# Optimization experiments

Hardware: AMD Instinct MI355X
Metric: run time of the kernel (lower is better)

The kernel has to match this reference:

```python
import jax, jax.numpy as jnp
import numpy as np

N_NODE = 2000
N_EDGE = 100000
N_REL2 = 102  # num_relation * 2
D_IN = 64
N_TRI = 500000


def _triangles(src, dst, N):
    """Faithful numpy port of triangle_list: for each edge (a,c) intersect
    out-neighbors of a with in-neighbors of c via sorted edge lists + searchsorted.
    Returns (edge_ab, edge_bc, edge_ac) edge-index triples."""
    E = len(src)
    src = src.astype(np.int64); dst = dst.astype(np.int64)
    in_order = np.argsort(src * N + dst, kind='stable')   # edges sorted by (a,b)
    out_order = np.argsort(dst * N + src, kind='stable')  # edges sorted by (c,b)
    deg_in = np.bincount(src, minlength=N)
    deg_out = np.bincount(dst, minlength=N)
    neighbor_out = dst[in_order]
    neighbor_in = src[out_order]
    cum_in = np.concatenate([[0], np.cumsum(deg_in)])
    cum_out = np.concatenate([[0], np.cumsum(deg_out)])
    # candidate b's: out-neighbors of a, replicated per edge (a,c)
    cnt_a = deg_in[src]
    ce = np.repeat(np.arange(E), cnt_a)
    offs = np.arange(cnt_a.sum()) - np.repeat(np.cumsum(cnt_a) - cnt_a, cnt_a)
    pos = np.repeat(cum_in[src], cnt_a) + offs
    b = neighbor_out[pos]
    ab_cand = in_order[pos]
    # boundary: in-neighbors of c, replicated per edge (globally sorted via N*segment offset)
    cnt_c = deg_out[dst]
    se = np.repeat(np.arange(E), cnt_c)
    offs2 = np.arange(cnt_c.sum()) - np.repeat(np.cumsum(cnt_c) - cnt_c, cnt_c)
    pos2 = np.repeat(cum_out[dst], cnt_c) + offs2
    boundary = neighbor_in[pos2] + N * se
    bc_order = out_order[pos2]
    key = b + N * ce
    left = np.searchsorted(boundary, key, side='left')
    right = np.searchsorted(boundary, key, side='right')
    count = right - left
    rep = np.repeat(np.arange(len(count)), count)
    within = np.arange(count.sum()) - np.repeat(np.cumsum(count) - count, count)
    return ab_cand[rep], bc_order[left[rep] + within], ce[rep]


def setup_inputs() -> dict:
    rng = np.random.default_rng(0)
    src = rng.integers(0, N_NODE, N_EDGE)
    dst = rng.integers(0, N_NODE, N_EDGE)
    edge_type = rng.integers(0, N_REL2, N_EDGE)
    ab, bc, ac = _triangles(src, dst, N_NODE)
    if len(ab) == 0:  # pathological fallback
        ab = rng.integers(0, N_EDGE, N_TRI)
        bc = rng.integers(0, N_EDGE, N_TRI)
        ac = rng.integers(0, N_EDGE, N_TRI)
    sel = rng.integers(0, len(ab), N_TRI)  # fixed-size (re)sample of triangles
    s = 0.1
    return {
        'edge_type': jnp.asarray(edge_type, jnp.int64) if jax.config.jax_enable_x64 else jnp.asarray(edge_type, jnp.int32),
        'edge_ab': jnp.asarray(ab[sel], jnp.int32),
        'edge_bc': jnp.asarray(bc[sel], jnp.int32),
        'edge_ac': jnp.asarray(ac[sel], jnp.int32),
        'fact_emb': jnp.asarray(rng.standard_normal((N_REL2, D_IN)) * s, jnp.float32),
        'W1': jnp.asarray(rng.standard_normal((D_IN, D_IN)) * s, jnp.float32),
        'b1': jnp.zeros((D_IN,), jnp.float32),
        'W2': jnp.asarray(rng.standard_normal((D_IN, D_IN)) * s, jnp.float32),
        'b2': jnp.zeros((D_IN,), jnp.float32),
        'mlp_W1': jnp.asarray(rng.standard_normal((2 * D_IN, 2 * D_IN)) * s, jnp.float32),
        'mlp_b1': jnp.zeros((2 * D_IN,), jnp.float32),
        'mlp_W2': jnp.asarray(rng.standard_normal((2 * D_IN, 1)) * s, jnp.float32),
        'mlp_b2': jnp.zeros((1,), jnp.float32),
    }


def reference(edge_type, edge_ab, edge_bc, edge_ac, fact_emb,
              W1, b1, W2, b2, mlp_W1, mlp_b1, mlp_W2, mlp_b2):
    E = edge_type.shape[0]
    x0 = fact_emb[edge_type]                      # [E, d] initial edge (fact) features
    x = x0
    for W, b in ((W1, b1), (W2, b2)):
        msg = x[edge_ab] * x[edge_bc]             # [T, d] distmult triangle messages
        agg = jax.ops.segment_sum(msg, edge_ac, num_segments=E)  # scatter-add onto ac edge
        x = jax.nn.relu(agg @ W + b)              # per-layer linear + activation
    feat = jnp.concatenate([x, x0], axis=-1)      # [E, 2d] (hidden + input, concat_hidden=False)
    h = jax.nn.relu(feat @ mlp_W1 + mlp_b1)
    return (h @ mlp_W2 + mlp_b2)[:, 0]            # [E] per-edge score
```

## Files before the change

kernel.cpp:

```cpp
#include <hip/hip_runtime.h>

#define D 64

__device__ __forceinline__ float relu_f(float v) { return v > 0.f ? v : 0.f; }


__global__ void k_hist(const int* __restrict__ ac, int* __restrict__ cnt, int T) {
    int t = blockIdx.x * blockDim.x + threadIdx.x;
    if (t < T) atomicAdd(&cnt[ac[t]], 1);
}

__global__ __launch_bounds__(256) void k_scanA(const int* __restrict__ cnt,
        int* __restrict__ localExcl, int* __restrict__ blockSums, int E) {
    __shared__ int ls[256];
    const int tid = threadIdx.x;
    int base = blockIdx.x * 1024 + tid * 4;
    int a0 = 0, a1 = 0, a2 = 0, a3 = 0;
    if (base + 3 < E) {
        int4 v = *reinterpret_cast<const int4*>(cnt + base);
        a0 = v.x; a1 = v.y; a2 = v.z; a3 = v.w;
    } else {
        if (base + 0 < E) a0 = cnt[base + 0];
        if (base + 1 < E) a1 = cnt[base + 1];
        if (base + 2 < E) a2 = cnt[base + 2];
        if (base + 3 < E) a3 = cnt[base + 3];
    }
    int tsum = a0 + a1 + a2 + a3;
    ls[tid] = tsum;
    __syncthreads();
    for (int off = 1; off < 256; off <<= 1) {
        int v = (tid >= off) ? ls[tid - off] : 0;
        __syncthreads();
        ls[tid] += v;
        __syncthreads();
    }
    int excl = ls[tid] - tsum;
    if (tid == 255) blockSums[blockIdx.x] = ls[255];
    if (base + 3 < E) {
        int4 o = make_int4(excl, excl + a0, excl + a0 + a1, excl + a0 + a1 + a2);
        *reinterpret_cast<int4*>(localExcl + base) = o;
    } else {
        int run = excl;
        if (base + 0 < E) { localExcl[base + 0] = run; run += a0; }
        if (base + 1 < E) { localExcl[base + 1] = run; run += a1; }
        if (base + 2 < E) { localExcl[base + 2] = run; run += a2; }
        if (base + 3 < E) { localExcl[base + 3] = run; }
    }
}

__global__ __launch_bounds__(256) void k_scanC(const int* __restrict__ localExcl,
        const int* __restrict__ blockSums, const int* __restrict__ cnt,
        int2* __restrict__ seg, int* __restrict__ cursor, int E, int nblk) {
    __shared__ int ls[256];
    const int tid = threadIdx.x;
    int v = (tid < nblk) ? blockSums[tid] : 0;
    ls[tid] = v;
    __syncthreads();
    for (int off = 1; off < 256; off <<= 1) {
        int w = (tid >= off) ? ls[tid - off] : 0;
        __syncthreads();
        ls[tid] += w;
        __syncthreads();
    }
    int excl = ls[tid] - v;
    __syncthreads();
    ls[tid] = excl;
    __syncthreads();
    int i = blockIdx.x * blockDim.x + tid;
    if (i < E) {
        int s = localExcl[i] + ls[i >> 10];
        seg[i] = make_int2(s, cnt[i]);
        cursor[i] = s;
    }
}

__global__ void k_permute(const int* __restrict__ ab, const int* __restrict__ bc,
                          const int* __restrict__ ac, const int* __restrict__ et,
                          int* __restrict__ cursor, int2* __restrict__ tri,
                          int* __restrict__ pid, int T, int nrel) {
    int t = blockIdx.x * blockDim.x + threadIdx.x;
    if (t >= T) return;
    int a = ab[t], b = bc[t];
    int pos = atomicAdd(&cursor[ac[t]], 1);
    tri[pos] = make_int2(a, b);
    pid[pos] = et[a] * nrel + et[b];
}

#define FPAD 65
__global__ __launch_bounds__(256) void k_pair(const float* __restrict__ fe,
        const float* __restrict__ W1, float* __restrict__ P, int nrel) {
    __shared__ float Wl[64 * 64];
    __shared__ float fT[64 * FPAD];
    const int npair = nrel * nrel;
    const int tid = threadIdx.x;
    const int p0 = blockIdx.x * 64;

    for (int i = tid; i < 1024; i += 256)
        reinterpret_cast<float4*>(Wl)[i] = reinterpret_cast<const float4*>(W1)[i];

    for (int i = tid; i < 1024; i += 256) {
        int r = i >> 4, q = i & 15;
        int p = p0 + r;
        float4 v = make_float4(0.f, 0.f, 0.f, 0.f);
        if (p < npair) {
            int pa = p / nrel, pb = p - pa * nrel;
            float4 va = reinterpret_cast<const float4*>(fe + (size_t)pa * D)[q];
            float4 vb = reinterpret_cast<const float4*>(fe + (size_t)pb * D)[q];
            v = make_float4(va.x * vb.x, va.y * vb.y, va.z * vb.z, va.w * vb.w);
        }
        fT[(q * 4 + 0) * FPAD + r] = v.x;
        fT[(q * 4 + 1) * FPAD + r] = v.y;
        fT[(q * 4 + 2) * FPAD + r] = v.z;
        fT[(q * 4 + 3) * FPAD + r] = v.w;
    }
    __syncthreads();

    const int j0 = (tid & 15) * 4;
    const int r0 = (tid >> 4) * 4;
    float acc[4][4];
    #pragma unroll
    for (int i = 0; i < 4; ++i)
        #pragma unroll
        for (int j = 0; j < 4; ++j) acc[i][j] = 0.f;

    #pragma unroll 8
    for (int k = 0; k < 64; ++k) {
        float4 f = *reinterpret_cast<const float4*>(&fT[k * FPAD + r0]);
        float4 w = *reinterpret_cast<const float4*>(&Wl[k * 64 + j0]);
        float fa[4] = {f.x, f.y, f.z, f.w};
        float wa[4] = {w.x, w.y, w.z, w.w};
        #pragma unroll
        for (int i = 0; i < 4; ++i)
            #pragma unroll
            for (int j = 0; j < 4; ++j) acc[i][j] += fa[i] * wa[j];
    }

    #pragma unroll
    for (int i = 0; i < 4; ++i) {
        int p = p0 + r0 + i;
        if (p < npair) {
            float4 o = make_float4(acc[i][0], acc[i][1], acc[i][2], acc[i][3]);
            *reinterpret_cast<float4*>(P + (size_t)p * D + j0) = o;
        }
    }
}

__global__ __launch_bounds__(128) void k_qtab(const float* __restrict__ fe,
        const float* __restrict__ mW1, const float* __restrict__ mb1,
        float* __restrict__ Q) {
    __shared__ float fl[64];
    const int t = blockIdx.x;
    const int j = threadIdx.x;
    if (j < 64) fl[j] = fe[(size_t)t * D + j];
    __syncthreads();
    float s = mb1[j];
    #pragma unroll 16
    for (int k = 0; k < 64; ++k)
        s += fl[k] * mW1[(size_t)(64 + k) * 128 + j];
    Q[(size_t)t * 128 + j] = s;
}

__global__ __launch_bounds__(256) void k_msg1b(const int2* __restrict__ seg,
        const int* __restrict__ pid, const float* __restrict__ P,
        const float* __restrict__ b1, float* __restrict__ xb, int E, int nquad) {
    const int tid = threadIdx.x;
    const int lane = tid & 63;
    const int sub = lane & 15;
    const int grp = lane >> 4;
    const float4* __restrict__ P4 = reinterpret_cast<const float4*>(P);
    const float4 bb = reinterpret_cast<const float4*>(b1)[sub];

    for (int quad = (blockIdx.x * blockDim.x + tid) >> 6; quad * 4 < E; quad += nquad) {
        const int e = quad * 4 + grp;
        int2 sc = make_int2(0, 0);
        if (e < E) sc = seg[e];
        const int s = sc.x, c = sc.y;
        float4 acc = make_float4(0.f, 0.f, 0.f, 0.f);
        int i = 0;
        for (; i + 3 < c; i += 4) {
            int q0 = pid[s + i + 0];
            int q1 = pid[s + i + 1];
            int q2 = pid[s + i + 2];
            int q3 = pid[s + i + 3];
            float4 v0 = P4[(size_t)q0 * 16 + sub];
            float4 v1 = P4[(size_t)q1 * 16 + sub];
            float4 v2 = P4[(size_t)q2 * 16 + sub];
            float4 v3 = P4[(size_t)q3 * 16 + sub];
            acc.x += v0.x + v1.x + v2.x + v3.x;
            acc.y += v0.y + v1.y + v2.y + v3.y;
            acc.z += v0.z + v1.z + v2.z + v3.z;
            acc.w += v0.w + v1.w + v2.w + v3.w;
        }
        for (; i < c; ++i) {
            float4 v = P4[(size_t)pid[s + i] * 16 + sub];
            acc.x += v.x; acc.y += v.y; acc.z += v.z; acc.w += v.w;
        }
        if (e < E) {
            float4 o;
            o.x = relu_f(acc.x + bb.x);
            o.y = relu_f(acc.y + bb.y);
            o.z = relu_f(acc.z + bb.z);
            o.w = relu_f(acc.w + bb.w);
            reinterpret_cast<float4*>(xb + (size_t)e * D)[sub] = o;
        }
    }
}

__global__ __launch_bounds__(256) void k_msg4(const int2* __restrict__ seg,
        const int2* __restrict__ tri, const float* __restrict__ xin,
        float* __restrict__ agg, int E, int nquad) {
    const int tid = threadIdx.x;
    const int lane = tid & 63;
    const int sub = lane & 15;
    const int grp = lane >> 4;
    const float4* __restrict__ x4 = reinterpret_cast<const float4*>(xin);

    for (int quad = (blockIdx.x * blockDim.x + tid) >> 6; quad * 4 < E; quad += nquad) {
        const int e = quad * 4 + grp;
        int2 sc = make_int2(0, 0);
        if (e < E) sc = seg[e];
        const int s = sc.x, c = sc.y;
        float4 acc = make_float4(0.f, 0.f, 0.f, 0.f);
        int i = 0;
        for (; i + 3 < c; i += 4) {
            int2 p0 = tri[s + i + 0];
            int2 p1 = tri[s + i + 1];
            int2 p2 = tri[s + i + 2];
            int2 p3 = tri[s + i + 3];
            float4 va0 = x4[(size_t)p0.x * 16 + sub];
            float4 vb0 = x4[(size_t)p0.y * 16 + sub];
            float4 va1 = x4[(size_t)p1.x * 16 + sub];
            float4 vb1 = x4[(size_t)p1.y * 16 + sub];
            float4 va2 = x4[(size_t)p2.x * 16 + sub];
            float4 vb2 = x4[(size_t)p2.y * 16 + sub];
            float4 va3 = x4[(size_t)p3.x * 16 + sub];
            float4 vb3 = x4[(size_t)p3.y * 16 + sub];
            acc.x += va0.x * vb0.x; acc.y += va0.y * vb0.y;
            acc.z += va0.z * vb0.z; acc.w += va0.w * vb0.w;
            acc.x += va1.x * vb1.x; acc.y += va1.y * vb1.y;
            acc.z += va1.z * vb1.z; acc.w += va1.w * vb1.w;
            acc.x += va2.x * vb2.x; acc.y += va2.y * vb2.y;
            acc.z += va2.z * vb2.z; acc.w += va2.w * vb2.w;
            acc.x += va3.x * vb3.x; acc.y += va3.y * vb3.y;
            acc.z += va3.z * vb3.z; acc.w += va3.w * vb3.w;
        }
        for (; i < c; ++i) {
            int2 p = tri[s + i];
            float4 va = x4[(size_t)p.x * 16 + sub];
            float4 vb = x4[(size_t)p.y * 16 + sub];
            acc.x += va.x * vb.x;
            acc.y += va.y * vb.y;
            acc.z += va.z * vb.z;
            acc.w += va.w * vb.w;
        }
        if (e < E)
            reinterpret_cast<float4*>(agg + (size_t)e * D)[sub] = acc;
    }
}

__global__ __launch_bounds__(256) void k_linear(const float* __restrict__ in,
        const float* __restrict__ W, const float* __restrict__ b,
        float* __restrict__ outx, int E) {
    __shared__ float Wl[64 * 64];
    __shared__ float fT[64 * FPAD];
    const int tid = threadIdx.x;
    const int row0 = blockIdx.x * 64;

    for (int i = tid; i < 1024; i += 256)
        reinterpret_cast<float4*>(Wl)[i] = reinterpret_cast<const float4*>(W)[i];

    for (int i = tid; i < 1024; i += 256) {
        int r = i >> 4, q = i & 15;
        float4 v = make_float4(0.f, 0.f, 0.f, 0.f);
        if (row0 + r < E)
            v = reinterpret_cast<const float4*>(in + (size_t)(row0 + r) * D)[q];
        fT[(q * 4 + 0) * FPAD + r] = v.x;
        fT[(q * 4 + 1) * FPAD + r] = v.y;
        fT[(q * 4 + 2) * FPAD + r] = v.z;
        fT[(q * 4 + 3) * FPAD + r] = v.w;
    }
    __syncthreads();

    const int j0 = (tid & 15) * 4;
    const int r0 = (tid >> 4) * 4;
    float acc[4][4];
    #pragma unroll
    for (int i = 0; i < 4; ++i)
        #pragma unroll
        for (int j = 0; j < 4; ++j) acc[i][j] = 0.f;

    #pragma unroll 8
    for (int k = 0; k < 64; ++k) {
        float4 f = *reinterpret_cast<const float4*>(&fT[k * FPAD + r0]);
        float4 w = *reinterpret_cast<const float4*>(&Wl[k * 64 + j0]);
        float fa[4] = {f.x, f.y, f.z, f.w};
        float wa[4] = {w.x, w.y, w.z, w.w};
        #pragma unroll
        for (int i = 0; i < 4; ++i)
            #pragma unroll
            for (int j = 0; j < 4; ++j) acc[i][j] += fa[i] * wa[j];
    }

    float4 bv = *reinterpret_cast<const float4*>(&b[j0]);
    float ba[4] = {bv.x, bv.y, bv.z, bv.w};
    #pragma unroll
    for (int i = 0; i < 4; ++i) {
        int row = row0 + r0 + i;
        if (row < E) {
            float4 o;
            o.x = relu_f(acc[i][0] + ba[0]);
            o.y = relu_f(acc[i][1] + ba[1]);
            o.z = relu_f(acc[i][2] + ba[2]);
            o.w = relu_f(acc[i][3] + ba[3]);
            *reinterpret_cast<float4*>(outx + (size_t)row * D + j0) = o;
        }
    }
}

#define MPAD 129
__global__ __launch_bounds__(512) void k_mlp(const float* __restrict__ x,
        const int* __restrict__ et, const float* __restrict__ Q,
        const float* __restrict__ W1, const float* __restrict__ W2,
        const float* __restrict__ b2, float* __restrict__ out, int E) {
    __shared__ float Wl[32 * 128];
    __shared__ float fT[32 * MPAD];
    __shared__ float W2l[128];
    const int tid = threadIdx.x;
    const int row0 = blockIdx.x * 128;

    if (tid < 128) W2l[tid] = W2[tid];

    const int jt = tid & 31;
    const int j0 = jt * 4;
    const int r0 = (tid >> 5) * 8;
    float acc[8][4];
    #pragma unroll
    for (int i = 0; i < 8; ++i)
        #pragma unroll
        for (int j = 0; j < 4; ++j) acc[i][j] = 0.f;

    for (int h = 0; h < 2; ++h) {
        __syncthreads();
        for (int i = tid; i < 1024; i += 512)
            reinterpret_cast<float4*>(Wl)[i] =
                reinterpret_cast<const float4*>(W1 + (size_t)h * 32 * 128)[i];
        for (int i = tid; i < 1024; i += 512) {
            int r = i >> 3, q = i & 7;
            int row = row0 + r;
            float4 v = make_float4(0.f, 0.f, 0.f, 0.f);
            if (row < E)
                v = reinterpret_cast<const float4*>(x + (size_t)row * D)[h * 8 + q];
            int kb = q * 4;
            fT[(kb + 0) * MPAD + r] = v.x;
            fT[(kb + 1) * MPAD + r] = v.y;
            fT[(kb + 2) * MPAD + r] = v.z;
            fT[(kb + 3) * MPAD + r] = v.w;
        }
        __syncthreads();

        #pragma unroll 4
        for (int k = 0; k < 32; ++k) {
            float4 fA = *reinterpret_cast<const float4*>(&fT[k * MPAD + r0]);
            float4 fB = *reinterpret_cast<const float4*>(&fT[k * MPAD + r0 + 4]);
            float4 w = *reinterpret_cast<const float4*>(&Wl[k * 128 + j0]);
            float fa[8] = {fA.x, fA.y, fA.z, fA.w, fB.x, fB.y, fB.z, fB.w};
            float wa[4] = {w.x, w.y, w.z, w.w};
            #pragma unroll
            for (int i = 0; i < 8; ++i)
                #pragma unroll
                for (int j = 0; j < 4; ++j) acc[i][j] += fa[i] * wa[j];
        }
    }

    float4 w2 = *reinterpret_cast<const float4*>(&W2l[j0]);
    float bias2 = b2[0];
    #pragma unroll
    for (int i = 0; i < 8; ++i) {
        int row = row0 + r0 + i;
        float4 qv = make_float4(0.f, 0.f, 0.f, 0.f);
        if (row < E)
            qv = reinterpret_cast<const float4*>(Q + (size_t)et[row] * 128)[jt];
        float h0 = relu_f(acc[i][0] + qv.x);
        float h1 = relu_f(acc[i][1] + qv.y);
        float h2 = relu_f(acc[i][2] + qv.z);
        float h3 = relu_f(acc[i][3] + qv.w);
        float p = h0 * w2.x + h1 * w2.y + h2 * w2.z + h3 * w2.w;
        #pragma unroll
        for (int m = 1; m < 32; m <<= 1) p += __shfl_xor(p, m, 64);
        if (jt == 0 && row < E) out[row] = p + bias2;
    }
}

extern "C" void kernel_launch(void* const* d_in, const int* in_sizes, int n_in,
                              void* d_out, int out_size, void* d_ws, size_t ws_size,
                              hipStream_t stream) {
    const int*   edge_type = (const int*)d_in[0];
    const int*   ab        = (const int*)d_in[1];
    const int*   bc        = (const int*)d_in[2];
    const int*   ac        = (const int*)d_in[3];
    const float* fe        = (const float*)d_in[4];
    const float* W1        = (const float*)d_in[5];
    const float* b1        = (const float*)d_in[6];
    const float* W2        = (const float*)d_in[7];
    const float* b2        = (const float*)d_in[8];
    const float* mW1       = (const float*)d_in[9];
    const float* mb1       = (const float*)d_in[10];
    const float* mW2       = (const float*)d_in[11];
    const float* mb2       = (const float*)d_in[12];

    const int E = in_sizes[0];
    const int T = in_sizes[1];
    const int nrel = in_sizes[4] / D;
    const int npair = nrel * nrel;
    float* out = (float*)d_out;

    char* p = (char*)d_ws;
    float* xa   = (float*)p;   p += (size_t)E * D * sizeof(float);
    float* xb   = (float*)p;   p += (size_t)E * D * sizeof(float);
    float* agg  = (float*)p;   p += (size_t)E * D * sizeof(float);
    float* P    = (float*)p;   p += (size_t)npair * D * sizeof(float);
    float* Q    = (float*)p;   p += (size_t)nrel * 128 * sizeof(float);
    int* cnt    = (int*)p;     p += (size_t)E * sizeof(int);
    int* lexcl  = (int*)p;     p += (size_t)E * sizeof(int);
    int* cursor = (int*)p;     p += (size_t)E * sizeof(int);
    int* bsums  = (int*)p;     p += 256 * sizeof(int);
    int2* seg   = (int2*)p;    p += (size_t)E * sizeof(int2);
    int2* tri   = (int2*)p;    p += (size_t)T * sizeof(int2);
    int* pid    = (int*)p;     p += (size_t)T * sizeof(int);

    const int nblkA = (E + 1023) / 1024;

    hipMemsetAsync(cnt, 0, (size_t)E * sizeof(int), stream);
    k_hist<<<(T + 255) / 256, 256, 0, stream>>>(ac, cnt, T);
    k_pair<<<(npair + 63) / 64, 256, 0, stream>>>(fe, W1, P, nrel);
    k_qtab<<<nrel, 128, 0, stream>>>(fe, mW1, mb1, Q);
    k_scanA<<<nblkA, 256, 0, stream>>>(cnt, lexcl, bsums, E);
    k_scanC<<<(E + 255) / 256, 256, 0, stream>>>(lexcl, bsums, cnt, seg, cursor, E, nblkA);
    k_permute<<<(T + 255) / 256, 256, 0, stream>>>(ab, bc, ac, edge_type, cursor, tri, pid, T, nrel);

    const int MSG_BLOCKS = 2048;
    const int nquad = MSG_BLOCKS * 256 / 64;
    k_msg1b<<<MSG_BLOCKS, 256, 0, stream>>>(seg, pid, P, b1, xb, E, nquad);
    k_msg4<<<MSG_BLOCKS, 256, 0, stream>>>(seg, tri, xb, agg, E, nquad);
    k_linear<<<(E + 63) / 64, 256, 0, stream>>>(agg, W2, b2, xa, E);

    k_mlp<<<(E + 127) / 128, 512, 0, stream>>>(xa, edge_type, Q, mW1, mW2, mb2, out, E);
}
```

Measured before the change: 182.9 us.

## Fuse setup kernels into one prep launch and merge layer-2 linear with MLP

Replaces the memset, pair-table and Q-table launches with a single block-partitioned prep kernel. It also fuses the second-layer linear with the final MLP, so the hidden activations stay in shared memory instead of being written to and re-read from a global buffer. This removes three launches and one E×64 float round trip through global memory. In exchange the fused kernel runs extra sequential GEMM phases with more syncs per block, and uses 64-row tiles instead of the previous 128-row MLP tiles.

Result: faster. 164.4 us (-10.2%).

```diff
diff --git a/kernel.cpp b/kernel.cpp
--- a/kernel.cpp
+++ b/kernel.cpp
@@ -1,8 +1,98 @@
 #include <hip/hip_runtime.h>
 
 #define D 64
+#define FPAD 65
 
 __device__ __forceinline__ float relu_f(float v) { return v > 0.f ? v : 0.f; }
+
+__global__ __launch_bounds__(256) void k_prep(int* __restrict__ cnt, int En,
+        const float* __restrict__ fe, const float* __restrict__ W1,
+        float* __restrict__ P, int nrel,
+        const float* __restrict__ mW1, const float* __restrict__ mb1,
+        float* __restrict__ Q, int nZ, int nP) {
+    __shared__ float Wl[64 * 64];
+    __shared__ float fT[64 * FPAD];
+    const int tid = threadIdx.x;
+    int b = blockIdx.x;
+
+    if (b < nZ) {
+        int i = (b * 256 + tid) * 4;
+        if (i + 3 < En) {
+            *reinterpret_cast<int4*>(cnt + i) = make_int4(0, 0, 0, 0);
+        } else {
+            for (int k = i; k < En; ++k) cnt[k] = 0;
+        }
+        return;
+    }
+    b -= nZ;
+    if (b < nP) {
+        const int npair = nrel * nrel;
+        const int p0 = b * 64;
+
+        for (int i = tid; i < 1024; i += 256)
+            reinterpret_cast<float4*>(Wl)[i] = reinterpret_cast<const float4*>(W1)[i];
+
+        for (int i = tid; i < 1024; i += 256) {
+            int r = i >> 4, q = i & 15;
+            int p = p0 + r;
+            float4 v = make_float4(0.f, 0.f, 0.f, 0.f);
+            if (p < npair) {
+                int pa = p / nrel, pb = p - pa * nrel;
+                float4 va = reinterpret_cast<const float4*>(fe + (size_t)pa * D)[q];
+                float4 vb = reinterpret_cast<const float4*>(fe + (size_t)pb * D)[q];
+                v = make_float4(va.x * vb.x, va.y * vb.y, va.z * vb.z, va.w * vb.w);
+            }
+            fT[(q * 4 + 0) * FPAD + r] = v.x;
+            fT[(q * 4 + 1) * FPAD + r] = v.y;
+            fT[(q * 4 + 2) * FPAD + r] = v.z;
+            fT[(q * 4 + 3) * FPAD + r] = v.w;
+        }
+        __syncthreads();
+
+        const int j0 = (tid & 15) * 4;
+        const int r0 = (tid >> 4) * 4;
+        float acc[4][4];
+        #pragma unroll
+        for (int i = 0; i < 4; ++i)
+            #pragma unroll
+            for (int j = 0; j < 4; ++j) acc[i][j] = 0.f;
+
+        #pragma unroll 8
+        for (int k = 0; k < 64; ++k) {
+            float4 f = *reinterpret_cast<const float4*>(&fT[k * FPAD + r0]);
+            float4 w = *reinterpret_cast<const float4*>(&Wl[k * 64 + j0]);
+            float fa[4] = {f.x, f.y, f.z, f.w};
+            float wa[4] = {w.x, w.y, w.z, w.w};
+            #pragma unroll
+            for (int i = 0; i < 4; ++i)
+                #pragma unroll
+                for (int j = 0; j < 4; ++j) acc[i][j] += fa[i] * wa[j];
+        }
+
+        #pragma unroll
+        for (int i = 0; i < 4; ++i) {
+            int p = p0 + r0 + i;
+            if (p < npair) {
+                float4 o = make_float4(acc[i][0], acc[i][1], acc[i][2], acc[i][3]);
+                *reinterpret_cast<float4*>(P + (size_t)p * D + j0) = o;
+            }
+        }
+        return;
+    }
+    b -= nP;
+    int t = b * 2 + (tid >> 7);
+    int j = tid & 127;
+    float* fl = &fT[(tid >> 7) * 64];
+    if (t < nrel && j < 64) fl[j] = fe[(size_t)t * D + j];
+    __syncthreads();
+    if (t < nrel) {
+        float s = mb1[j];
+        #pragma unroll 16
+        for (int k = 0; k < 64; ++k)
+            s += fl[k] * mW1[(size_t)(64 + k) * 128 + j];
+        Q[(size_t)t * 128 + j] = s;
+    }
+}
 
 
 __global__ void k_hist(const int* __restrict__ ac, int* __restrict__ cnt, int T) {
@@ -84,80 +174,6 @@
     int pos = atomicAdd(&cursor[ac[t]], 1);
     tri[pos] = make_int2(a, b);
     pid[pos] = et[a] * nrel + et[b];
-}
-
-#define FPAD 65
-__global__ __launch_bounds__(256) void k_pair(const float* __restrict__ fe,
-        const float* __restrict__ W1, float* __restrict__ P, int nrel) {
-    __shared__ float Wl[64 * 64];
-    __shared__ float fT[64 * FPAD];
-    const int npair = nrel * nrel;
-    const int tid = threadIdx.x;
-    const int p0 = blockIdx.x * 64;
-
-    for (int i = tid; i < 1024; i += 256)
-        reinterpret_cast<float4*>(Wl)[i] = reinterpret_cast<const float4*>(W1)[i];
-
-    for (int i = tid; i < 1024; i += 256) {
-        int r = i >> 4, q = i & 15;
-        int p = p0 + r;
-        float4 v = make_float4(0.f, 0.f, 0.f, 0.f);
-        if (p < npair) {
-            int pa = p / nrel, pb = p - pa * nrel;
-            float4 va = reinterpret_cast<const float4*>(fe + (size_t)pa * D)[q];
-            float4 vb = reinterpret_cast<const float4*>(fe + (size_t)pb * D)[q];
-            v = make_float4(va.x * vb.x, va.y * vb.y, va.z * vb.z, va.w * vb.w);
-        }
-        fT[(q * 4 + 0) * FPAD + r] = v.x;
-        fT[(q * 4 + 1) * FPAD + r] = v.y;
-        fT[(q * 4 + 2) * FPAD + r] = v.z;
-        fT[(q * 4 + 3) * FPAD + r] = v.w;
-    }
-    __syncthreads();
-
-    const int j0 = (tid & 15) * 4;
-    const int r0 = (tid >> 4) * 4;
-    float acc[4][4];
-    #pragma unroll
-    for (int i = 0; i < 4; ++i)
-        #pragma unroll
-        for (int j = 0; j < 4; ++j) acc[i][j] = 0.f;
-
-    #pragma unroll 8
-    for (int k = 0; k < 64; ++k) {
-        float4 f = *reinterpret_cast<const float4*>(&fT[k * FPAD + r0]);
-        float4 w = *reinterpret_cast<const float4*>(&Wl[k * 64 + j0]);
-        float fa[4] = {f.x, f.y, f.z, f.w};
-        float wa[4] = {w.x, w.y, w.z, w.w};
-        #pragma unroll
-        for (int i = 0; i < 4; ++i)
-            #pragma unroll
-            for (int j = 0; j < 4; ++j) acc[i][j] += fa[i] * wa[j];
-    }
-
-    #pragma unroll
-    for (int i = 0; i < 4; ++i) {
-        int p = p0 + r0 + i;
-        if (p < npair) {
-            float4 o = make_float4(acc[i][0], acc[i][1], acc[i][2], acc[i][3]);
-            *reinterpret_cast<float4*>(P + (size_t)p * D + j0) = o;
-        }
-    }
-}
-
-__global__ __launch_bounds__(128) void k_qtab(const float* __restrict__ fe,
-        const float* __restrict__ mW1, const float* __restrict__ mb1,
-        float* __restrict__ Q) {
-    __shared__ float fl[64];
-    const int t = blockIdx.x;
-    const int j = threadIdx.x;
-    if (j < 64) fl[j] = fe[(size_t)t * D + j];
-    __syncthreads();
-    float s = mb1[j];
-    #pragma unroll 16
-    for (int k = 0; k < 64; ++k)
-        s += fl[k] * mW1[(size_t)(64 + k) * 128 + j];
-    Q[(size_t)t * 128 + j] = s;
 }
 
 __global__ __launch_bounds__(256) void k_msg1b(const int2* __restrict__ seg,
@@ -258,22 +274,25 @@
     }
 }
 
-__global__ __launch_bounds__(256) void k_linear(const float* __restrict__ in,
-        const float* __restrict__ W, const float* __restrict__ b,
-        float* __restrict__ outx, int E) {
+__global__ __launch_bounds__(256) void k_linmlp(const float* __restrict__ agg,
+        const int* __restrict__ et, const float* __restrict__ Q,
+        const float* __restrict__ W2, const float* __restrict__ b2,
+        const float* __restrict__ mW1, const float* __restrict__ mW2,
+        const float* __restrict__ mb2, float* __restrict__ out, int E) {
     __shared__ float Wl[64 * 64];
     __shared__ float fT[64 * FPAD];
     const int tid = threadIdx.x;
     const int row0 = blockIdx.x * 64;
+    const int j0 = (tid & 15) * 4;
+    const int r0 = (tid >> 4) * 4;
 
     for (int i = tid; i < 1024; i += 256)
-        reinterpret_cast<float4*>(Wl)[i] = reinterpret_cast<const float4*>(W)[i];
-
+        reinterpret_cast<float4*>(Wl)[i] = reinterpret_cast<const float4*>(W2)[i];
     for (int i = tid; i < 1024; i += 256) {
         int r = i >> 4, q = i & 15;
         float4 v = make_float4(0.f, 0.f, 0.f, 0.f);
         if (row0 + r < E)
-            v = reinterpret_cast<const float4*>(in + (size_t)(row0 + r) * D)[q];
+            v = reinterpret_cast<const float4*>(agg + (size_t)(row0 + r) * D)[q];
         fT[(q * 4 + 0) * FPAD + r] = v.x;
         fT[(q * 4 + 1) * FPAD + r] = v.y;
         fT[(q * 4 + 2) * FPAD + r] = v.z;
@@ -281,8 +300,6 @@
     }
     __syncthreads();
 
-    const int j0 = (tid & 15) * 4;
-    const int r0 = (tid >> 4) * 4;
     float acc[4][4];
     #pragma unroll
     for (int i = 0; i < 4; ++i)
@@ -301,93 +318,112 @@
             for (int j = 0; j < 4; ++j) acc[i][j] += fa[i] * wa[j];
     }
 
-    float4 bv = *reinterpret_cast<const float4*>(&b[j0]);
-    float ba[4] = {bv.x, bv.y, bv.z, bv.w};
+    {
+        float4 bv = *reinterpret_cast<const float4*>(&b2[j0]);
+        float ba[4] = {bv.x, bv.y, bv.z, bv.w};
+        #pragma unroll
+        for (int i = 0; i < 4; ++i)
+            #pragma unroll
+            for (int j = 0; j < 4; ++j) acc[i][j] = relu_f(acc[i][j] + ba[j]);
+    }
+
+    __syncthreads();
+
+    #pragma unroll
+    for (int i = 0; i < 4; ++i)
+        #pragma unroll
+        for (int j = 0; j < 4; ++j)
+            fT[(j0 + j) * FPAD + (r0 + i)] = acc[i][j];
+    for (int i = tid; i < 1024; i += 256) {
+        int k = i >> 4, q = i & 15;
+        reinterpret_cast<float4*>(Wl)[i] =
+            *reinterpret_cast<const float4*>(mW1 + (size_t)k * 128 + q * 4);
+    }
+    __syncthreads();
+
+    int etc_[4];
     #pragma unroll
     for (int i = 0; i < 4; ++i) {
         int row = row0 + r0 + i;
-        if (row < E) {
-            float4 o;
-            o.x = relu_f(acc[i][0] + ba[0]);
-            o.y = relu_f(acc[i][1] + ba[1]);
-            o.z = relu_f(acc[i][2] + ba[2]);
-            o.w = relu_f(acc[i][3] + ba[3]);
-            *reinterpret_cast<float4*>(outx + (size_t)row * D + j0) = o;
-        }
-    }
-}
-
-#define MPAD 129
-__global__ __launch_bounds__(512) void k_mlp(const float* __restrict__ x,
-        const int* __restrict__ et, const float* __restrict__ Q,
-        const float* __restrict__ W1, const float* __restrict__ W2,
-        const float* __restrict__ b2, float* __restrict__ out, int E) {
-    __shared__ float Wl[32 * 128];
-    __shared__ float fT[32 * MPAD];
-    __shared__ float W2l[128];
-    const int tid = threadIdx.x;
-    const int row0 = blockIdx.x * 128;
-
-    if (tid < 128) W2l[tid] = W2[tid];
-
-    const int jt = tid & 31;
-    const int j0 = jt * 4;
-    const int r0 = (tid >> 5) * 8;
-    float acc[8][4];
+        etc_[i] = (row < E) ? et[row] : 0;
+    }
+
+    float p[4] = {0.f, 0.f, 0.f, 0.f};
+
+    {
+        float acc2[4][4];
+        #pragma unroll
+        for (int i = 0; i < 4; ++i)
+            #pragma unroll
+            for (int j = 0; j < 4; ++j) acc2[i][j] = 0.f;
+        #pragma unroll 8
+        for (int k = 0; k < 64; ++k) {
+            float4 f = *reinterpret_cast<const float4*>(&fT[k * FPAD + r0]);
+            float4 w = *reinterpret_cast<const float4*>(&Wl[k * 64 + j0]);
+            float fa[4] = {f.x, f.y, f.z, f.w};
+            float wa[4] = {w.x, w.y, w.z, w.w};
+            #pragma unroll
+            for (int i = 0; i < 4; ++i)
+                #pragma unroll
+                for (int j = 0; j < 4; ++j) acc2[i][j] += fa[i] * wa[j];
+        }
+        float4 w2v = *reinterpret_cast<const float4*>(&mW2[j0]);
+        #pragma unroll
+        for (int i = 0; i < 4; ++i) {
+            float4 qv = *reinterpret_cast<const float4*>(&Q[(size_t)etc_[i] * 128 + j0]);
+            p[i] += relu_f(acc2[i][0] + qv.x) * w2v.x;
+            p[i] += relu_f(acc2[i][1] + qv.y) * w2v.y;
+            p[i] += relu_f(acc2[i][2] + qv.z) * w2v.z;
+            p[i] += relu_f(acc2[i][3] + qv.w) * w2v.w;
+        }
+    }
+    __syncthreads();
+    for (int i = tid; i < 1024; i += 256) {
+        int k = i >> 4, q = i & 15;
+        reinterpret_cast<float4*>(Wl)[i] =
+            *reinterpret_cast<const float4*>(mW1 + (size_t)k * 128 + 64 + q * 4);
+    }
+    __syncthreads();
+    {
+        float acc2[4][4];
+        #pragma unroll
+        for (int i = 0; i < 4; ++i)
+            #pragma unroll
+            for (int j = 0; j < 4; ++j) acc2[i][j] = 0.f;
+        #pragma unroll 8
+        for (int k = 0; k < 64; ++k) {
+            float4 f = *reinterpret_cast<const float4*>(&fT[k * FPAD + r0]);
+            float4 w = *reinterpret_cast<const float4*>(&Wl[k * 64 + j0]);
+            float fa[4] = {f.x, f.y, f.z, f.w};
+            float wa[4] = {w.x, w.y, w.z, w.w};
+            #pragma unroll
+            for (int i = 0; i < 4; ++i)
+                #pragma unroll
+                for (int j = 0; j < 4; ++j) acc2[i][j] += fa[i] * wa[j];
+        }
+        float4 w2v = *reinterpret_cast<const float4*>(&mW2[64 + j0]);
+        #pragma unroll
+        for (int i = 0; i < 4; ++i) {
+            float4 qv = *reinterpret_cast<const float4*>(&Q[(size_t)etc_[i] * 128 + 64 + j0]);
+            p[i] += relu_f(acc2[i][0] + qv.x) * w2v.x;
+            p[i] += relu_f(acc2[i][1] + qv.y) * w2v.y;
+            p[i] += relu_f(acc2[i][2] + qv.z) * w2v.z;
+            p[i] += relu_f(acc2[i][3] + qv.w) * w2v.w;
+        }
+    }
+
+    const float bias2 = mb2[0];
     #pragma unroll
-    for (int i = 0; i < 8; ++i)
-        #pragma unroll
-        for (int j = 0; j < 4; ++j) acc[i][j] = 0.f;
-
-    for (int h = 0; h < 2; ++h) {
-        __syncthreads();
-        for (int i = tid; i < 1024; i += 512)
-            reinterpret_cast<float4*>(Wl)[i] =
-                reinterpret_cast<const float4*>(W1 + (size_t)h * 32 * 128)[i];
-        for (int i = tid; i < 1024; i += 512) {
-            int r = i >> 3, q = i & 7;
-            int row = row0 + r;
-            float4 v = make_float4(0.f, 0.f, 0.f, 0.f);
-            if (row < E)
-                v = reinterpret_cast<const float4*>(x + (size_t)row * D)[h * 8 + q];
-            int kb = q * 4;
-            fT[(kb + 0) * MPAD + r] = v.x;
-            fT[(kb + 1) * MPAD + r] = v.y;
-            fT[(kb + 2) * MPAD + r] = v.z;
-            fT[(kb + 3) * MPAD + r] = v.w;
-        }
-        __syncthreads();
-
-        #pragma unroll 4
-        for (int k = 0; k < 32; ++k) {
-            float4 fA = *reinterpret_cast<const float4*>(&fT[k * MPAD + r0]);
-            float4 fB = *reinterpret_cast<const float4*>(&fT[k * MPAD + r0 + 4]);
-            float4 w = *reinterpret_cast<const float4*>(&Wl[k * 128 + j0]);
-            float fa[8] = {fA.x, fA.y, fA.z, fA.w, fB.x, fB.y, fB.z, fB.w};
-            float wa[4] = {w.x, w.y, w.z, w.w};
-            #pragma unroll
-            for (int i = 0; i < 8; ++i)
-                #pragma unroll
-                for (int j = 0; j < 4; ++j) acc[i][j] += fa[i] * wa[j];
-        }
-    }
-
-    float4 w2 = *reinterpret_cast<const float4*>(&W2l[j0]);
-    float bias2 = b2[0];
-    #pragma unroll
-    for (int i = 0; i < 8; ++i) {
-        int row = row0 + r0 + i;
-        float4 qv = make_float4(0.f, 0.f, 0.f, 0.f);
-        if (row < E)
-            qv = reinterpret_cast<const float4*>(Q + (size_t)et[row] * 128)[jt];
-        float h0 = relu_f(acc[i][0] + qv.x);
-        float h1 = relu_f(acc[i][1] + qv.y);
-        float h2 = relu_f(acc[i][2] + qv.z);
-        float h3 = relu_f(acc[i][3] + qv.w);
-        float p = h0 * w2.x + h1 * w2.y + h2 * w2.z + h3 * w2.w;
-        #pragma unroll
-        for (int m = 1; m < 32; m <<= 1) p += __shfl_xor(p, m, 64);
-        if (jt == 0 && row < E) out[row] = p + bias2;
+    for (int i = 0; i < 4; ++i) {
+        float s = p[i];
+        s += __shfl_xor(s, 1, 64);
+        s += __shfl_xor(s, 2, 64);
+        s += __shfl_xor(s, 4, 64);
+        s += __shfl_xor(s, 8, 64);
+        if ((tid & 15) == 0) {
+            int row = row0 + r0 + i;
+            if (row < E) out[row] = s + bias2;
+        }
     }
 }
 
@@ -415,7 +451,6 @@
     float* out = (float*)d_out;
 
     char* p = (char*)d_ws;
-    float* xa   = (float*)p;   p += (size_t)E * D * sizeof(float);
     float* xb   = (float*)p;   p += (size_t)E * D * sizeof(float);
     float* agg  = (float*)p;   p += (size_t)E * D * sizeof(float);
     float* P    = (float*)p;   p += (size_t)npair * D * sizeof(float);
@@ -429,11 +464,12 @@
     int* pid    = (int*)p;     p += (size_t)T * sizeof(int);
 
     const int nblkA = (E + 1023) / 1024;
-
-    hipMemsetAsync(cnt, 0, (size_t)E * sizeof(int), stream);
+    const int nZ = (E + 1023) / 1024;
+    const int nP = (npair + 63) / 64;
+    const int nQb = (nrel + 1) / 2;
+
+    k_prep<<<nZ + nP + nQb, 256, 0, stream>>>(cnt, E, fe, W1, P, nrel, mW1, mb1, Q, nZ, nP);
     k_hist<<<(T + 255) / 256, 256, 0, stream>>>(ac, cnt, T);
-    k_pair<<<(npair + 63) / 64, 256, 0, stream>>>(fe, W1, P, nrel);
-    k_qtab<<<nrel, 128, 0, stream>>>(fe, mW1, mb1, Q);
     k_scanA<<<nblkA, 256, 0, stream>>>(cnt, lexcl, bsums, E);
     k_scanC<<<(E + 255) / 256, 256, 0, stream>>>(lexcl, bsums, cnt, seg, cursor, E, nblkA);
     k_permute<<<(T + 255) / 256, 256, 0, stream>>>(ab, bc, ac, edge_type, cursor, tri, pid, T, nrel);
@@ -442,7 +478,5 @@
     const int nquad = MSG_BLOCKS * 256 / 64;
     k_msg1b<<<MSG_BLOCKS, 256, 0, stream>>>(seg, pid, P, b1, xb, E, nquad);
     k_msg4<<<MSG_BLOCKS, 256, 0, stream>>>(seg, tri, xb, agg, E, nquad);
-    k_linear<<<(E + 63) / 64, 256, 0, stream>>>(agg, W2, b2, xa, E);
-
-    k_mlp<<<(E + 127) / 128, 512, 0, stream>>>(xa, edge_type, Q, mW1, mW2, mb2, out, E);
-}
+    k_linmlp<<<(E + 63) / 64, 256, 0, stream>>>(agg, edge_type, Q, W2, b2, mW1, mW2, mb2, out, E);
+}
```
